# Kernel optimization log

Hardware: AMD Instinct MI355X
Metric: run time of the kernel (lower is better)

The kernel has to match this reference:

```python
import jax, jax.numpy as jnp
import numpy as np

N, D_IN, D_OUT = 2048, 256, 64
ALPHA = 0.2  # LeakyReLU slope
LN_EPS = 1e-5


def setup_inputs() -> dict:
    key = jax.random.key(0)
    ks = jax.random.split(key, 8)
    features = jax.random.normal(ks[0], (N, D_IN), dtype=jnp.float32)
    adj = jax.random.randint(ks[1], (N, N), 0, 2, dtype=jnp.int32)
    adj = adj.at[jnp.arange(N), jnp.arange(N)].set(1)  # self-loops: no all-masked rows
    s_in = 1.0 / np.sqrt(D_IN)
    s_out = 1.0 / np.sqrt(D_OUT)
    phi_w = jax.random.uniform(ks[2], (D_OUT, D_IN), jnp.float32, -s_in, s_in)
    phi_b = jax.random.uniform(ks[3], (D_OUT,), jnp.float32, -s_in, s_in)
    mu_w = jax.random.uniform(ks[4], (D_OUT,), jnp.float32, -s_out, s_out)
    mu_b = jax.random.uniform(ks[5], (), jnp.float32, -s_out, s_out)
    ln_g = jnp.ones((D_OUT,), jnp.float32)
    ln_b = jnp.zeros((D_OUT,), jnp.float32)
    return {"features": features, "adj": adj, "phi_w": phi_w, "phi_b": phi_b,
            "ln_g": ln_g, "ln_b": ln_b, "mu_w": mu_w, "mu_b": mu_b}


def _layernorm(x, g, b):
    mu = jnp.mean(x, axis=-1, keepdims=True)
    var = jnp.mean(jnp.square(x - mu), axis=-1, keepdims=True)
    return (x - mu) * jax.lax.rsqrt(var + LN_EPS) * g + b


def reference(features, adj, phi_w, phi_b, ln_g, ln_b, mu_w, mu_b):
    h = features @ phi_w.T + phi_b           # [N, D_OUT]
    h = _layernorm(h, ln_g, ln_b)
    # v2 path: scores[i,j,:] = h[i] + h[j]; e = mu(scores)
    scores = h[:, None, :] + h[None, :, :]   # [N, N, D_OUT]
    e = jnp.einsum('ijd,d->ij', scores, mu_w) + mu_b  # [N, N]
    e = jax.nn.leaky_relu(e, ALPHA)          # activation applied after if/else
    e = jnp.where(adj == 0, -jnp.inf, e)
    a = jax.nn.softmax(e, axis=1)            # dropout p=0 -> identity
    return jax.nn.elu(a @ h)                 # [N, D_OUT]
```

## Files before the change

### kernel.cpp

```cpp
#include <hip/hip_runtime.h>
#include <hip/hip_bf16.h>

#define N_ROWS 2048
#define D_IN   256
#define D_OUT  64
#define JSLAB  8
#define ALPHA  0.2f
#define LN_EPS 1e-5f

typedef __attribute__((ext_vector_type(4))) float f32x4;
typedef __attribute__((ext_vector_type(8))) short s16x8;

static __device__ __forceinline__ unsigned short f2bf(float x) {
    unsigned u = __float_as_uint(x);
    unsigned r = (u + 0x7FFFu + ((u >> 16) & 1u)) >> 16;
    return (unsigned short)r;
}
static __device__ __forceinline__ float bf2f(unsigned short u) {
    return __uint_as_float(((unsigned)u) << 16);
}

__global__ __launch_bounds__(256) void k1_h_s(
    const float* __restrict__ F, const float* __restrict__ phiW,
    const float* __restrict__ phiB, const float* __restrict__ lnG,
    const float* __restrict__ lnB, const float* __restrict__ muW,
    float* __restrict__ s_buf, unsigned short* __restrict__ HhiT,
    unsigned short* __restrict__ HloT)
{
    __shared__ f32x4 phiS[64 * 64];
    __shared__ unsigned short Thi[64][8];
    __shared__ unsigned short Tlo[64][8];

    const int tid  = threadIdx.x;
    const int w    = tid >> 6;
    const int lane = tid & 63;
    const int i_base = blockIdx.x * 8;
    const int r0 = i_base + w * 2;

    const f32x4* phiW4 = (const f32x4*)phiW;
    const f32x4* F4    = (const f32x4*)F;

    #pragma unroll
    for (int t = 0; t < 16; ++t) {
        int idx = tid + t * 256;
        int d = idx >> 6, g = idx & 63;
        phiS[(d << 6) | ((g + d) & 63)] = phiW4[idx];
    }
    __syncthreads();

    float acc[2] = {0.f, 0.f};
    #pragma unroll 8
    for (int g = 0; g < 64; ++g) {
        f32x4 p = phiS[(lane << 6) | ((g + lane) & 63)];
        #pragma unroll
        for (int rr = 0; rr < 2; ++rr) {
            f32x4 f = F4[(r0 + rr) * 64 + g];
            acc[rr] += p.x * f.x + p.y * f.y + p.z * f.z + p.w * f.w;
        }
    }

    const float pb = phiB[lane], gg = lnG[lane], bb = lnB[lane], mw = muW[lane];

    #pragma unroll
    for (int rr = 0; rr < 2; ++rr) {
        float h = acc[rr] + pb;
        float m = h;
        #pragma unroll
        for (int off = 32; off >= 1; off >>= 1) m += __shfl_xor(m, off);
        m *= (1.f / 64.f);
        float c = h - m;
        float v = c * c;
        #pragma unroll
        for (int off = 32; off >= 1; off >>= 1) v += __shfl_xor(v, off);
        v *= (1.f / 64.f);
        float hn = c * rsqrtf(v + LN_EPS) * gg + bb;
        float sp = hn * mw;
        #pragma unroll
        for (int off = 32; off >= 1; off >>= 1) sp += __shfl_xor(sp, off);
        if (lane == 0) s_buf[r0 + rr] = sp;
        unsigned short hi = f2bf(hn);
        unsigned short lo = f2bf(hn - bf2f(hi));
        Thi[lane][w * 2 + rr] = hi;
        Tlo[lane][w * 2 + rr] = lo;
    }
    __syncthreads();
    if (tid < 128) {
        int d = tid >> 1, half = tid & 1;
        ushort4 vh = *(const ushort4*)&Thi[d][half * 4];
        *(ushort4*)&HhiT[d * N_ROWS + i_base + half * 4] = vh;
        ushort4 vl = *(const ushort4*)&Tlo[d][half * 4];
        *(ushort4*)&HloT[d * N_ROWS + i_base + half * 4] = vl;
    }
}

__global__ __launch_bounds__(256) void k2_attn(
    const int* __restrict__ adj, const float* __restrict__ s_buf,
    const unsigned short* __restrict__ HhiT, const unsigned short* __restrict__ HloT,
    const float* __restrict__ muB,
    float* __restrict__ numP, float* __restrict__ l_p)
{
    __shared__ __align__(16) unsigned short Wt[4][16][72];
    __shared__ f32x4 cN[4][4][64];
    __shared__ f32x4 cL[4][64];

    const int tid  = threadIdx.x;
    const int w    = tid >> 6;
    const int lane = tid & 63;
    const int stripe = blockIdx.x >> 3;
    const int slab   = blockIdx.x & 7;
    const int i0 = stripe * 16;
    const int jb = slab * 256 + w * 64;
    const float mub = muB[0];

    const int rsel = lane & 15;
    const int rsub = lane >> 4;

    f32x4 accN[4];
    f32x4 accL;
    #pragma unroll
    for (int nb = 0; nb < 4; ++nb) { accN[nb][0]=0.f; accN[nb][1]=0.f; accN[nb][2]=0.f; accN[nb][3]=0.f; }
    accL[0]=0.f; accL[1]=0.f; accL[2]=0.f; accL[3]=0.f;

    s16x8 ones;
    #pragma unroll
    for (int e = 0; e < 8; ++e) ones[e] = (short)0x3F80;

    const float4 sj4 = ((const float4*)s_buf)[(jb >> 2) + rsel];
    const int4* adj4 = (const int4*)adj;
    #pragma unroll
    for (int r4 = 0; r4 < 4; ++r4) {
        const int row = r4 * 4 + rsub;
        const int i = i0 + row;
        const float si = s_buf[i];
        int4 a = adj4[(size_t)i * (N_ROWS / 4) + (jb >> 2) + rsel];
        ushort4 pk;
        { float z = si + sj4.x + mub; float e = z > 0.f ? z : ALPHA * z; pk.x = a.x ? f2bf(__expf(e)) : 0; }
        { float z = si + sj4.y + mub; float e = z > 0.f ? z : ALPHA * z; pk.y = a.y ? f2bf(__expf(e)) : 0; }
        { float z = si + sj4.z + mub; float e = z > 0.f ? z : ALPHA * z; pk.z = a.z ? f2bf(__expf(e)) : 0; }
        { float z = si + sj4.w + mub; float e = z > 0.f ? z : ALPHA * z; pk.w = a.w ? f2bf(__expf(e)) : 0; }
        *(ushort4*)&Wt[w][row][rsel * 4] = pk;
    }

    s16x8 a0 = *(const s16x8*)&Wt[w][rsel][rsub * 8];
    s16x8 a1 = *(const s16x8*)&Wt[w][rsel][32 + rsub * 8];

    accL = __builtin_amdgcn_mfma_f32_16x16x32_bf16(a0, ones, accL, 0, 0, 0);
    accL = __builtin_amdgcn_mfma_f32_16x16x32_bf16(a1, ones, accL, 0, 0, 0);
    #pragma unroll
    for (int nb = 0; nb < 4; ++nb) {
        const unsigned short* hr = HhiT + (size_t)(nb * 16 + rsel) * N_ROWS + jb + rsub * 8;
        s16x8 b0 = *(const s16x8*)hr;
        s16x8 b1 = *(const s16x8*)(hr + 32);
        accN[nb] = __builtin_amdgcn_mfma_f32_16x16x32_bf16(a0, b0, accN[nb], 0, 0, 0);
        accN[nb] = __builtin_amdgcn_mfma_f32_16x16x32_bf16(a1, b1, accN[nb], 0, 0, 0);
        const unsigned short* lr = HloT + (size_t)(nb * 16 + rsel) * N_ROWS + jb + rsub * 8;
        s16x8 c0 = *(const s16x8*)lr;
        s16x8 c1 = *(const s16x8*)(lr + 32);
        accN[nb] = __builtin_amdgcn_mfma_f32_16x16x32_bf16(a0, c0, accN[nb], 0, 0, 0);
        accN[nb] = __builtin_amdgcn_mfma_f32_16x16x32_bf16(a1, c1, accN[nb], 0, 0, 0);
    }

    #pragma unroll
    for (int nb = 0; nb < 4; ++nb) cN[w][nb][lane] = accN[nb];
    cL[w][lane] = accL;
    __syncthreads();

    {
        f32x4 n = cN[0][w][lane] + cN[1][w][lane] + cN[2][w][lane] + cN[3][w][lane];
        float* np = numP + (size_t)slab * (N_ROWS * D_OUT);
        #pragma unroll
        for (int r = 0; r < 4; ++r)
            np[(i0 + rsub * 4 + r) * D_OUT + w * 16 + rsel] = n[r];
    }
    if (w == 0) {
        f32x4 l = cL[0][lane] + cL[1][lane] + cL[2][lane] + cL[3][lane];
        if (rsel == 0) {
            #pragma unroll
            for (int r = 0; r < 4; ++r)
                l_p[stripe * 128 + slab * 16 + rsub * 4 + r] = l[r];
        }
    }
}

__global__ __launch_bounds__(256) void k3_combine(
    const float* __restrict__ numP, const float* __restrict__ l_p,
    float* __restrict__ out)
{
    const int idx = (blockIdx.x * 256 + threadIdx.x) * 4;
    const int row = idx >> 6;
    const int stripe = row >> 4;
    const int r = row & 15;
    f32x4 n = {0.f, 0.f, 0.f, 0.f};
    float l = 0.f;
    #pragma unroll
    for (int sl = 0; sl < JSLAB; ++sl) {
        n += *(const f32x4*)(numP + (size_t)sl * (N_ROWS * D_OUT) + idx);
        l += l_p[stripe * 128 + sl * 16 + r];
    }
    const float inv = 1.f / l;
    f32x4 o;
    #pragma unroll
    for (int e = 0; e < 4; ++e) {
        float v = n[e] * inv;
        o[e] = v > 0.f ? v : expm1f(v);
    }
    *(f32x4*)&out[idx] = o;
}

extern "C" void kernel_launch(void* const* d_in, const int* in_sizes, int n_in,
                              void* d_out, int out_size, void* d_ws, size_t ws_size,
                              hipStream_t stream)
{
    const float* F    = (const float*)d_in[0];
    const int*   adj  = (const int*)d_in[1];
    const float* phiW = (const float*)d_in[2];
    const float* phiB = (const float*)d_in[3];
    const float* lnG  = (const float*)d_in[4];
    const float* lnB  = (const float*)d_in[5];
    const float* muW  = (const float*)d_in[6];
    const float* muB  = (const float*)d_in[7];
    float* out = (float*)d_out;

    float* ws   = (float*)d_ws;
    float* s    = ws;
    float* l_p  = ws + N_ROWS;
    float* numP = l_p + 128 * 128;
    unsigned short* HhiT = (unsigned short*)(numP + (size_t)JSLAB * N_ROWS * D_OUT);
    unsigned short* HloT = HhiT + (size_t)D_OUT * N_ROWS;

    k1_h_s<<<dim3(256), dim3(256), 0, stream>>>(F, phiW, phiB, lnG, lnB, muW,
                                                s, HhiT, HloT);
    k2_attn<<<dim3(128 * JSLAB), dim3(256), 0, stream>>>(adj, s, HhiT, HloT, muB,
                                                         numP, l_p);
    k3_combine<<<dim3(128), dim3(256), 0, stream>>>(numP, l_p, out);
}
```

Measured before the change: 28.77 us.

## Fuse combine kernel into attention kernel with full-row blocks and in-block reduction

Each attention block now owns 8 full rows, and its 8 waves each walk 256 columns in 4 software-pipelined iterations that prefetch the next adjacency tile. The per-slab partial numerators and row sums are reduced in shared memory, and the normalisation and ELU are applied in the same kernel. This drops the third launch and the global round trip through the partial buffers. The cost is that half of each 16-row MFMA tile is zero padding, so matrix work per useful row doubles, and there are fewer blocks (256) with a longer serial loop per wave.

Result: slower. 32.97 us (+14.6%).

```diff
diff --git a/kernel.cpp b/kernel.cpp
--- a/kernel.cpp
+++ b/kernel.cpp
@@ -4,7 +4,6 @@
 #define N_ROWS 2048
 #define D_IN   256
 #define D_OUT  64
-#define JSLAB  8
 #define ALPHA  0.2f
 #define LN_EPS 1e-5f
 
@@ -93,28 +92,30 @@
     }
 }
 
-__global__ __launch_bounds__(256) void k2_attn(
+__global__ __launch_bounds__(512) void k2_attn(
     const int* __restrict__ adj, const float* __restrict__ s_buf,
     const unsigned short* __restrict__ HhiT, const unsigned short* __restrict__ HloT,
-    const float* __restrict__ muB,
-    float* __restrict__ numP, float* __restrict__ l_p)
+    const float* __restrict__ muB, float* __restrict__ out)
 {
-    __shared__ __align__(16) unsigned short Wt[4][16][72];
-    __shared__ f32x4 cN[4][4][64];
-    __shared__ f32x4 cL[4][64];
+    __shared__ __align__(16) unsigned short Wt[8][16][72];
+    __shared__ f32x4 cN[8][4][64];
+    __shared__ f32x4 cL[8][64];
 
     const int tid  = threadIdx.x;
     const int w    = tid >> 6;
     const int lane = tid & 63;
-    const int stripe = blockIdx.x >> 3;
-    const int slab   = blockIdx.x & 7;
-    const int i0 = stripe * 16;
-    const int jb = slab * 256 + w * 64;
+    const int i0 = blockIdx.x * 8;
     const float mub = muB[0];
 
     const int rsel = lane & 15;
     const int rsub = lane >> 4;
 
+    if (rsel >= 8) {
+        #pragma unroll
+        for (int z = 0; z < 18; ++z)
+            Wt[w][rsel][rsub * 18 + z] = 0;
+    }
+
     f32x4 accN[4];
     f32x4 accL;
     #pragma unroll
@@ -125,39 +126,58 @@
     #pragma unroll
     for (int e = 0; e < 8; ++e) ones[e] = (short)0x3F80;
 
-    const float4 sj4 = ((const float4*)s_buf)[(jb >> 2) + rsel];
     const int4* adj4 = (const int4*)adj;
-    #pragma unroll
-    for (int r4 = 0; r4 < 4; ++r4) {
-        const int row = r4 * 4 + rsub;
-        const int i = i0 + row;
-        const float si = s_buf[i];
-        int4 a = adj4[(size_t)i * (N_ROWS / 4) + (jb >> 2) + rsel];
-        ushort4 pk;
-        { float z = si + sj4.x + mub; float e = z > 0.f ? z : ALPHA * z; pk.x = a.x ? f2bf(__expf(e)) : 0; }
-        { float z = si + sj4.y + mub; float e = z > 0.f ? z : ALPHA * z; pk.y = a.y ? f2bf(__expf(e)) : 0; }
-        { float z = si + sj4.z + mub; float e = z > 0.f ? z : ALPHA * z; pk.z = a.z ? f2bf(__expf(e)) : 0; }
-        { float z = si + sj4.w + mub; float e = z > 0.f ? z : ALPHA * z; pk.w = a.w ? f2bf(__expf(e)) : 0; }
-        *(ushort4*)&Wt[w][row][rsel * 4] = pk;
-    }
-
-    s16x8 a0 = *(const s16x8*)&Wt[w][rsel][rsub * 8];
-    s16x8 a1 = *(const s16x8*)&Wt[w][rsel][32 + rsub * 8];
-
-    accL = __builtin_amdgcn_mfma_f32_16x16x32_bf16(a0, ones, accL, 0, 0, 0);
-    accL = __builtin_amdgcn_mfma_f32_16x16x32_bf16(a1, ones, accL, 0, 0, 0);
-    #pragma unroll
-    for (int nb = 0; nb < 4; ++nb) {
-        const unsigned short* hr = HhiT + (size_t)(nb * 16 + rsel) * N_ROWS + jb + rsub * 8;
-        s16x8 b0 = *(const s16x8*)hr;
-        s16x8 b1 = *(const s16x8*)(hr + 32);
-        accN[nb] = __builtin_amdgcn_mfma_f32_16x16x32_bf16(a0, b0, accN[nb], 0, 0, 0);
-        accN[nb] = __builtin_amdgcn_mfma_f32_16x16x32_bf16(a1, b1, accN[nb], 0, 0, 0);
-        const unsigned short* lr = HloT + (size_t)(nb * 16 + rsel) * N_ROWS + jb + rsub * 8;
-        s16x8 c0 = *(const s16x8*)lr;
-        s16x8 c1 = *(const s16x8*)(lr + 32);
-        accN[nb] = __builtin_amdgcn_mfma_f32_16x16x32_bf16(a0, c0, accN[nb], 0, 0, 0);
-        accN[nb] = __builtin_amdgcn_mfma_f32_16x16x32_bf16(a1, c1, accN[nb], 0, 0, 0);
+    const float si0 = s_buf[i0 + rsub];
+    const float si1 = s_buf[i0 + 4 + rsub];
+
+    int4 aNxt0 = adj4[(size_t)(i0 + rsub)     * (N_ROWS / 4) + ((w * 256) >> 2) + rsel];
+    int4 aNxt1 = adj4[(size_t)(i0 + 4 + rsub) * (N_ROWS / 4) + ((w * 256) >> 2) + rsel];
+
+    #pragma unroll
+    for (int it = 0; it < 4; ++it) {
+        const int jb = w * 256 + it * 64;
+        const float4 sj4 = ((const float4*)s_buf)[(jb >> 2) + rsel];
+        int4 a0v = aNxt0, a1v = aNxt1;
+        if (it < 3) {
+            const int jn = (jb + 64) >> 2;
+            aNxt0 = adj4[(size_t)(i0 + rsub)     * (N_ROWS / 4) + jn + rsel];
+            aNxt1 = adj4[(size_t)(i0 + 4 + rsub) * (N_ROWS / 4) + jn + rsel];
+        }
+        {
+            ushort4 pk;
+            { float z = si0 + sj4.x + mub; float e = z > 0.f ? z : ALPHA * z; pk.x = a0v.x ? f2bf(__expf(e)) : 0; }
+            { float z = si0 + sj4.y + mub; float e = z > 0.f ? z : ALPHA * z; pk.y = a0v.y ? f2bf(__expf(e)) : 0; }
+            { float z = si0 + sj4.z + mub; float e = z > 0.f ? z : ALPHA * z; pk.z = a0v.z ? f2bf(__expf(e)) : 0; }
+            { float z = si0 + sj4.w + mub; float e = z > 0.f ? z : ALPHA * z; pk.w = a0v.w ? f2bf(__expf(e)) : 0; }
+            *(ushort4*)&Wt[w][rsub][rsel * 4] = pk;
+        }
+        {
+            ushort4 pk;
+            { float z = si1 + sj4.x + mub; float e = z > 0.f ? z : ALPHA * z; pk.x = a1v.x ? f2bf(__expf(e)) : 0; }
+            { float z = si1 + sj4.y + mub; float e = z > 0.f ? z : ALPHA * z; pk.y = a1v.y ? f2bf(__expf(e)) : 0; }
+            { float z = si1 + sj4.z + mub; float e = z > 0.f ? z : ALPHA * z; pk.z = a1v.z ? f2bf(__expf(e)) : 0; }
+            { float z = si1 + sj4.w + mub; float e = z > 0.f ? z : ALPHA * z; pk.w = a1v.w ? f2bf(__expf(e)) : 0; }
+            *(ushort4*)&Wt[w][4 + rsub][rsel * 4] = pk;
+        }
+
+        s16x8 af0 = *(const s16x8*)&Wt[w][rsel][rsub * 8];
+        s16x8 af1 = *(const s16x8*)&Wt[w][rsel][32 + rsub * 8];
+
+        accL = __builtin_amdgcn_mfma_f32_16x16x32_bf16(af0, ones, accL, 0, 0, 0);
+        accL = __builtin_amdgcn_mfma_f32_16x16x32_bf16(af1, ones, accL, 0, 0, 0);
+        #pragma unroll
+        for (int nb = 0; nb < 4; ++nb) {
+            const unsigned short* hr = HhiT + (size_t)(nb * 16 + rsel) * N_ROWS + jb + rsub * 8;
+            s16x8 b0 = *(const s16x8*)hr;
+            s16x8 b1 = *(const s16x8*)(hr + 32);
+            accN[nb] = __builtin_amdgcn_mfma_f32_16x16x32_bf16(af0, b0, accN[nb], 0, 0, 0);
+            accN[nb] = __builtin_amdgcn_mfma_f32_16x16x32_bf16(af1, b1, accN[nb], 0, 0, 0);
+            const unsigned short* lr = HloT + (size_t)(nb * 16 + rsel) * N_ROWS + jb + rsub * 8;
+            s16x8 c0 = *(const s16x8*)lr;
+            s16x8 c1 = *(const s16x8*)(lr + 32);
+            accN[nb] = __builtin_amdgcn_mfma_f32_16x16x32_bf16(af0, c0, accN[nb], 0, 0, 0);
+            accN[nb] = __builtin_amdgcn_mfma_f32_16x16x32_bf16(af1, c1, accN[nb], 0, 0, 0);
+        }
     }
 
     #pragma unroll
@@ -165,46 +185,24 @@
     cL[w][lane] = accL;
     __syncthreads();
 
-    {
-        f32x4 n = cN[0][w][lane] + cN[1][w][lane] + cN[2][w][lane] + cN[3][w][lane];
-        float* np = numP + (size_t)slab * (N_ROWS * D_OUT);
-        #pragma unroll
-        for (int r = 0; r < 4; ++r)
-            np[(i0 + rsub * 4 + r) * D_OUT + w * 16 + rsel] = n[r];
-    }
-    if (w == 0) {
-        f32x4 l = cL[0][lane] + cL[1][lane] + cL[2][lane] + cL[3][lane];
-        if (rsel == 0) {
+    if (w < 4) {
+        f32x4 n = {0.f, 0.f, 0.f, 0.f};
+        f32x4 l = {0.f, 0.f, 0.f, 0.f};
+        #pragma unroll
+        for (int v = 0; v < 8; ++v) {
+            n += cN[v][w][lane];
+            l += cL[v][lane];
+        }
+        if (rsub < 2) {
             #pragma unroll
-            for (int r = 0; r < 4; ++r)
-                l_p[stripe * 128 + slab * 16 + rsub * 4 + r] = l[r];
-        }
-    }
-}
-
-__global__ __launch_bounds__(256) void k3_combine(
-    const float* __restrict__ numP, const float* __restrict__ l_p,
-    float* __restrict__ out)
-{
-    const int idx = (blockIdx.x * 256 + threadIdx.x) * 4;
-    const int row = idx >> 6;
-    const int stripe = row >> 4;
-    const int r = row & 15;
-    f32x4 n = {0.f, 0.f, 0.f, 0.f};
-    float l = 0.f;
-    #pragma unroll
-    for (int sl = 0; sl < JSLAB; ++sl) {
-        n += *(const f32x4*)(numP + (size_t)sl * (N_ROWS * D_OUT) + idx);
-        l += l_p[stripe * 128 + sl * 16 + r];
-    }
-    const float inv = 1.f / l;
-    f32x4 o;
-    #pragma unroll
-    for (int e = 0; e < 4; ++e) {
-        float v = n[e] * inv;
-        o[e] = v > 0.f ? v : expm1f(v);
-    }
-    *(f32x4*)&out[idx] = o;
+            for (int r = 0; r < 4; ++r) {
+                const int row = rsub * 4 + r;
+                float val = n[r] / l[r];
+                val = val > 0.f ? val : expm1f(val);
+                out[(i0 + row) * D_OUT + w * 16 + rsel] = val;
+            }
+        }
+    }
 }
 
 extern "C" void kernel_launch(void* const* d_in, const int* in_sizes, int n_in,
@@ -223,14 +221,10 @@
 
     float* ws   = (float*)d_ws;
     float* s    = ws;
-    float* l_p  = ws + N_ROWS;
-    float* numP = l_p + 128 * 128;
-    unsigned short* HhiT = (unsigned short*)(numP + (size_t)JSLAB * N_ROWS * D_OUT);
+    unsigned short* HhiT = (unsigned short*)(ws + N_ROWS);
     unsigned short* HloT = HhiT + (size_t)D_OUT * N_ROWS;
 
     k1_h_s<<<dim3(256), dim3(256), 0, stream>>>(F, phiW, phiB, lnG, lnB, muW,
                                                 s, HhiT, HloT);
-    k2_attn<<<dim3(128 * JSLAB), dim3(256), 0, stream>>>(adj, s, HhiT, HloT, muB,
-                                                         numP, l_p);
-    k3_combine<<<dim3(128), dim3(256), 0, stream>>>(numP, l_p, out);
-}
+    k2_attn<<<dim3(256), dim3(512), 0, stream>>>(adj, s, HhiT, HloT, muB, out);
+}
```
